# Performance work log

Measured on AMD Instinct MI355X. Metric: run time of the kernel, lower is better.

## Reference

```python
import jax, jax.numpy as jnp
import numpy as np

N = 768          # number of proposals (graph nodes)
C = 1024         # box_head feature dim (in_feats)
HC = 256         # RelPN hidden_c
K = 20           # topk edges per node
GH = 256         # gcn_hidden
H1 = 4           # gat1 heads
IMG_H, IMG_W = 800.0, 800.0
NEG_SLOPE = 0.2  # PyG GATConv leaky_relu slope


def setup_inputs() -> dict:
    key = jax.random.key(0)
    ks = jax.random.split(key, 24)
    s = 0.02
    feats = jax.random.normal(ks[0], (N, C), jnp.float32)
    # valid boxes inside an 800x800 image
    cx = jax.random.uniform(ks[1], (N,), minval=100.0, maxval=700.0)
    cy = jax.random.uniform(ks[2], (N,), minval=100.0, maxval=700.0)
    w = jax.random.uniform(ks[3], (N,), minval=10.0, maxval=200.0)
    h = jax.random.uniform(ks[4], (N,), minval=10.0, maxval=200.0)
    boxes = jnp.stack([cx - 0.5 * w, cy - 0.5 * h, cx + 0.5 * w, cy + 0.5 * h], axis=1)
    rn = lambda k, sh: jax.random.normal(k, sh, jnp.float32) * s
    return {
        'feats': feats, 'boxes': boxes,
        # RelationProposalNetwork: fc1(2C+4 -> HC), fc2(HC -> 1)
        'W1': rn(ks[5], (2 * C + 4, HC)), 'b1': jnp.zeros((HC,), jnp.float32),
        'W2': rn(ks[6], (HC, 1)), 'b2': jnp.zeros((1,), jnp.float32),
        # GATConv(C+4 -> GH, heads=4)
        'g1W': rn(ks[7], (C + 4, H1 * GH)), 'g1as': rn(ks[8], (H1, GH)),
        'g1ad': rn(ks[9], (H1, GH)), 'g1b': jnp.zeros((H1 * GH,), jnp.float32),
        # GATConv(GH*4 -> 2, heads=1)
        'g2W': rn(ks[10], (H1 * GH, 2)), 'g2as': rn(ks[11], (1, 2)),
        'g2ad': rn(ks[12], (1, 2)), 'g2b': jnp.zeros((2,), jnp.float32),
        'rW1': rn(ks[13], (H1 * GH + 4, GH // 2)), 'rb1': jnp.zeros((GH // 2,), jnp.float32),
        'rW2': rn(ks[14], (GH // 2, 4)), 'rb2': jnp.zeros((4,), jnp.float32),
    }


def _gat(xin, W, a_src, a_dst, bias, heads, feat, nbr):
    """PyG-style GATConv (eval mode, self-loops already in nbr). nbr: [N, K+1] src ids per dst."""
    n = xin.shape[0]
    xp = (xin @ W).reshape(n, heads, feat)              # [N,H,F]
    asrc = jnp.einsum('nhf,hf->nh', xp, a_src)          # [N,H]
    adst = jnp.einsum('nhf,hf->nh', xp, a_dst)          # [N,H]
    logits = jax.nn.leaky_relu(asrc[nbr] + adst[:, None, :], NEG_SLOPE)  # [N,K+1,H]
    alpha = jax.nn.softmax(logits, axis=1)              # softmax over incoming edges per dst
    out = jnp.einsum('nkh,nkhf->nhf', alpha, xp[nbr])   # gather + weighted aggregate
    return out.reshape(n, heads * feat) + bias


def reference(feats, boxes, W1, b1, W2, b2, g1W, g1as, g1ad, g1b,
              g2W, g2as, g2ad, g2b, rW1, rb1, rW2, rb2):
    n = feats.shape[0]
    scale = jnp.array([IMG_W, IMG_H, IMG_W, IMG_H], jnp.float32)
    geom = boxes / scale                                 # _box_geom: normalized coords
    x = jnp.concatenate([feats, geom], axis=1)           # [N, C+4]

    # --- RelationProposalNetwork: fc1(cat[f_i, f_j, |b_i - b_j|]) decomposed ---
    Wa, Wb, Wg = W1[:C], W1[C:2 * C], W1[2 * C:]
    fa = feats @ Wa                                      # i-part  [N,HC]
    fb = feats @ Wb                                      # j-part  [N,HC]
    gdiff = jnp.abs(boxes[:, None, :] - boxes[None, :, :])          # [N,N,4]
    h = jax.nn.relu(fa[:, None, :] + fb[None, :, :]
                    + jnp.einsum('ijd,dh->ijh', gdiff, Wg) + b1)    # [N,N,HC]
    rel = jnp.einsum('ijh,h->ij', h, W2[:, 0]) + b2[0]              # [N,N]

    # --- top-k edges per destination node (exclude self), plus self-loops ---
    rel_masked = jnp.where(jnp.eye(n, dtype=bool), -1e9, rel)
    _, nbr = jax.lax.top_k(rel_masked, K)                # [N,K] src j for each dst i
    nbr = jnp.concatenate([nbr, jnp.arange(n)[:, None]], axis=1)    # [N,K+1]

    # --- GAT propagation ---
    h1 = jax.nn.relu(_gat(x, g1W, g1as, g1ad, g1b, H1, GH, nbr))    # [N,1024]
    logits = _gat(h1, g2W, g2as, g2ad, g2b, 1, 2, nbr)              # [N,2]

    reg_in = jnp.concatenate([h1, geom], axis=1)
    delta = jax.nn.relu(reg_in @ rW1 + rb1) @ rW2 + rb2             # [N,4]
    px0, py0, px1, py1 = boxes[:, 0], boxes[:, 1], boxes[:, 2], boxes[:, 3]
    pw, ph = px1 - px0, py1 - py0
    pcx, pcy = px0 + 0.5 * pw, py0 + 0.5 * ph
    dx, dy, dw, dh = delta[:, 0], delta[:, 1], delta[:, 2], delta[:, 3]
    gcx, gcy = dx * pw + pcx, dy * ph + pcy
    gw, gh = jnp.exp(dw) * pw, jnp.exp(dh) * ph
    final_boxes = jnp.stack([gcx - 0.5 * gw, gcy - 0.5 * gh,
                             gcx + 0.5 * gw, gcy + 0.5 * gh], axis=1)
    return jnp.concatenate([logits, final_boxes], axis=1)  # [N,6]
```

## Files before the change

kernel.cpp:

```cpp
#include <hip/hip_runtime.h>
#include <math.h>

#define NN 768
#define KK_TOP 20
#define NBR_K 21

typedef __attribute__((ext_vector_type(8))) short bf16x8;
typedef __attribute__((ext_vector_type(4))) float f32x4;
typedef unsigned short ushort_t;
typedef unsigned int uint_t;

__device__ __forceinline__ ushort_t f2bf(float x) {
    union { float f; uint_t u; } c; c.f = x;
    uint_t r = (c.u + 0x7FFFu + ((c.u >> 16) & 1u)) >> 16;
    return (ushort_t)r;
}
__device__ __forceinline__ float bf2f(ushort_t u) {
    union { uint_t u; float f; } c; c.u = ((uint_t)u) << 16;
    return c.f;
}

struct Params {
    const float *feats, *boxes, *W1, *b1, *W2, *b2;
    const float *g1W, *g1as, *g1ad, *g1b, *g2W, *g2as, *g2ad, *g2b;
    const float *rW1, *rb1, *rW2, *rb2;
    float *out;
    float *fafb, *xp, *relm, *hid, *Arow, *Brow, *asrc, *adst, *xp2, *aux2;
    float4 *wgt4; float *w2p, *consts;
    float *va, *vb, *av;
    int *nbr;
    ushort_t *featsbf, *btAB, *btG, *btR, *h1bf;
};

__global__ __launch_bounds__(256) void k_prep(Params P)
{
    int b = blockIdx.x, t = threadIdx.x;
    if (b == 800) {
        const float* Wg = P.W1 + 2048 * 256;
        float q0 = Wg[t], q1 = Wg[256 + t], q2 = Wg[512 + t], q3 = Wg[768 + t];
        float w2 = P.W2[t];
        P.wgt4[t] = make_float4(q0, q1, q2, q3);
        P.w2p[t] = w2;
        __shared__ float red[256];
        float vals[5] = {q0 * w2, q1 * w2, q2 * w2, q3 * w2, P.b1[t] * w2};
        for (int d = 0; d < 5; d++) {
            red[t] = vals[d]; __syncthreads();
            for (int s = 128; s > 0; s >>= 1) {
                if (t < s) red[t] += red[t + s];
                __syncthreads();
            }
            if (t == 0) P.consts[d] = red[0];
            __syncthreads();
        }
        return;
    }
    if (b >= 1313) {
        int o = (b - 1313) * 4 + (t >> 6);
        int lane = t & 63;
        if (o >= 8224) return;
        int vec = o / 1028, k = o - vec * 1028;
        int h = vec & 3;
        const float4* aw = (const float4*)(((vec < 4) ? P.g1as : P.g1ad) + h * 256);
        const float4* gw = (const float4*)(P.g1W + (size_t)k * 1024 + h * 256);
        float4 a = aw[lane], g = gw[lane];
        float s = a.x * g.x + a.y * g.y + a.z * g.z + a.w * g.w;
#pragma unroll
        for (int off = 32; off > 0; off >>= 1) s += __shfl_xor(s, off);
        if (lane == 0) P.av[o] = s;
        return;
    }
    if (b >= 801) {
        int o = (b - 801) * 4 + (t >> 6);
        int lane = t & 63;
        const float4* row = (const float4*)(P.W1 + (size_t)o * 256);
        float4 w = ((const float4*)P.W2)[lane];
        float4 f = row[lane];
        float s = f.x * w.x + f.y * w.y + f.z * w.z + f.w * w.w;
#pragma unroll
        for (int off = 32; off > 0; off >>= 1) s += __shfl_xor(s, off);
        if (lane == 0) { if (o < 1024) P.va[o] = s; else P.vb[o - 1024] = s; }
        return;
    }
    if (b >= 416) {
        int gid = (b - 416) * 2048 + t * 8;
        float4 v0 = *(const float4*)(P.feats + gid);
        float4 v1 = *(const float4*)(P.feats + gid + 4);
        uint4 r;
        r.x = (uint_t)f2bf(v0.x) | ((uint_t)f2bf(v0.y) << 16);
        r.y = (uint_t)f2bf(v0.z) | ((uint_t)f2bf(v0.w) << 16);
        r.z = (uint_t)f2bf(v1.x) | ((uint_t)f2bf(v1.y) << 16);
        r.w = (uint_t)f2bf(v1.z) | ((uint_t)f2bf(v1.w) << 16);
        *(uint4*)(P.featsbf + gid) = r;
        return;
    }
    const float* in; ushort_t* out; int ldN, tk, tn;
    if (b < 64)       { in = P.W1;              out = P.btAB;              ldN = 256;  tn = b & 3;  tk = b >> 2; }
    else if (b < 128) { int i = b - 64;  in = P.W1 + 1024 * 256; out = P.btAB + 256 * 1024; ldN = 256;  tn = i & 3;  tk = i >> 2; }
    else if (b < 384) { int i = b - 128; in = P.g1W;             out = P.btG;               ldN = 1024; tn = i & 15; tk = i >> 4; }
    else              { int i = b - 384; in = P.rW1;             out = P.btR;               ldN = 128;  tn = i & 1;  tk = i >> 1; }

    __shared__ __align__(16) float tile[64][68];
    int k0 = tk * 64, n0 = tn * 64;
#pragma unroll
    for (int it = 0; it < 4; it++) {
        int r = (t >> 4) + it * 16;
        int c = (t & 15) * 4;
        *(float4*)&tile[r][c] = *(const float4*)(in + (size_t)(k0 + r) * ldN + n0 + c);
    }
    __syncthreads();
    int n = t >> 2;
    int kc = (t & 3) * 16;
    uint_t p[8];
#pragma unroll
    for (int h = 0; h < 8; h++) {
        ushort_t lo = f2bf(tile[kc + 2 * h][n]);
        ushort_t hi = f2bf(tile[kc + 2 * h + 1][n]);
        p[h] = (uint_t)lo | ((uint_t)hi << 16);
    }
    ushort_t* dst = out + (size_t)(n0 + n) * 1024 + k0 + kc;
    *(uint4*)dst = make_uint4(p[0], p[1], p[2], p[3]);
    *(uint4*)(dst + 8) = make_uint4(p[4], p[5], p[6], p[7]);
}

__device__ __forceinline__ void mfma_unit(
    int bx, int by, const ushort_t* __restrict__ A, const ushort_t* __restrict__ Bt,
    float* __restrict__ C, int ldc, int mode,
    const float* __restrict__ boxes, const float* __restrict__ Wgeo,
    const float* __restrict__ bias, int t, char* smem)
{
    ushort_t (*As)[72] = (ushort_t(*)[72])smem;
    ushort_t (*Bs)[72] = (ushort_t(*)[72])(smem + 64 * 72 * 2);
    int m0 = by * 64, n0 = bx * 64;
    int lane = t & 63, w = t >> 6;
    int quad = lane >> 4, ci = lane & 15;

    int r0 = t >> 3, q0 = t & 7;
    int r1 = (t + 256) >> 3, q1 = (t + 256) & 7;

    const ushort_t* Abase = A + (size_t)(m0 + r0) * 1024 + q0 * 8;
    const ushort_t* Abase1 = A + (size_t)(m0 + r1) * 1024 + q1 * 8;
    const ushort_t* Bbase = Bt + (size_t)(n0 + r0) * 1024 + q0 * 8;
    const ushort_t* Bbase1 = Bt + (size_t)(n0 + r1) * 1024 + q1 * 8;

    uint4 pa0 = *(const uint4*)(Abase);
    uint4 pa1 = *(const uint4*)(Abase1);
    uint4 pb0 = *(const uint4*)(Bbase);
    uint4 pb1 = *(const uint4*)(Bbase1);

    f32x4 acc[2][2];
    acc[0][0] = (f32x4){0.f, 0.f, 0.f, 0.f};
    acc[0][1] = (f32x4){0.f, 0.f, 0.f, 0.f};
    acc[1][0] = (f32x4){0.f, 0.f, 0.f, 0.f};
    acc[1][1] = (f32x4){0.f, 0.f, 0.f, 0.f};

    int arow = (w & 1) * 32 + ci;
    int brow = (w >> 1) * 32 + ci;

    for (int kt = 0; kt < 16; kt++) {
        *(uint4*)&As[r0][q0 * 8] = pa0;
        *(uint4*)&As[r1][q1 * 8] = pa1;
        *(uint4*)&Bs[r0][q0 * 8] = pb0;
        *(uint4*)&Bs[r1][q1 * 8] = pb1;
        __syncthreads();
        if (kt < 15) {
            int ko = (kt + 1) * 64;
            pa0 = *(const uint4*)(Abase + ko);
            pa1 = *(const uint4*)(Abase1 + ko);
            pb0 = *(const uint4*)(Bbase + ko);
            pb1 = *(const uint4*)(Bbase1 + ko);
        }
#pragma unroll
        for (int s = 0; s < 2; s++) {
            int kb = s * 32 + quad * 8;
            bf16x8 a0 = *(const bf16x8*)&As[arow][kb];
            bf16x8 a1 = *(const bf16x8*)&As[arow + 16][kb];
            bf16x8 b0 = *(const bf16x8*)&Bs[brow][kb];
            bf16x8 b1 = *(const bf16x8*)&Bs[brow + 16][kb];
            acc[0][0] = __builtin_amdgcn_mfma_f32_16x16x32_bf16(a0, b0, acc[0][0], 0, 0, 0);
            acc[0][1] = __builtin_amdgcn_mfma_f32_16x16x32_bf16(a0, b1, acc[0][1], 0, 0, 0);
            acc[1][0] = __builtin_amdgcn_mfma_f32_16x16x32_bf16(a1, b0, acc[1][0], 0, 0, 0);
            acc[1][1] = __builtin_amdgcn_mfma_f32_16x16x32_bf16(a1, b1, acc[1][1], 0, 0, 0);
        }
        __syncthreads();
    }

    const float inv800 = 1.0f / 800.0f;
#pragma unroll
    for (int ni = 0; ni < 2; ni++) {
        int col = n0 + (w >> 1) * 32 + ni * 16 + ci;
        float wg0 = 0.f, wg1 = 0.f, wg2 = 0.f, wg3 = 0.f, bv = 0.f;
        if (mode) {
            wg0 = Wgeo[col]; wg1 = Wgeo[ldc + col];
            wg2 = Wgeo[2 * ldc + col]; wg3 = Wgeo[3 * ldc + col];
            if (mode == 2) bv = bias[col];
        }
#pragma unroll
        for (int mi = 0; mi < 2; mi++) {
            int rbase = m0 + (w & 1) * 32 + mi * 16 + quad * 4;
#pragma unroll
            for (int reg = 0; reg < 4; reg++) {
                int row = rbase + reg;
                float v = acc[mi][ni][reg];
                if (mode) {
                    float4 bx4 = *(const float4*)(boxes + row * 4);
                    v += (bx4.x * wg0 + bx4.y * wg1 + bx4.z * wg2 + bx4.w * wg3) * inv800 + bv;
                    if (mode == 2) v = fmaxf(v, 0.f);
                }
                C[(size_t)row * ldc + col] = v;
            }
        }
    }
}

__global__ __launch_bounds__(256) void k_gemms(Params P)
{
    __shared__ __align__(16) char smem[18432];
    int u = blockIdx.x, t = threadIdx.x;
    if (u < 96) {
        mfma_unit(u & 7, u >> 3, P.featsbf, P.btAB, P.fafb, 512, 0,
                  nullptr, nullptr, nullptr, t, smem);
    } else if (u < 288) {
        int v = u - 96;
        mfma_unit(v & 15, v >> 4, P.featsbf, P.btG, P.xp, 1024, 1,
                  P.boxes, P.g1W + (size_t)1024 * 1024, nullptr, t, smem);
    } else if (u < 480) {
        int row = (u - 288) * 4 + (t >> 6);
        int lane = t & 63;
        const float4* fr = (const float4*)(P.feats + (size_t)row * 1024);
        const float4* va4 = (const float4*)P.va;
        const float4* vb4 = (const float4*)P.vb;
        float s1 = 0.f, s2 = 0.f;
#pragma unroll
        for (int it = 0; it < 4; it++) {
            int idx = it * 64 + lane;
            float4 f = fr[idx], a = va4[idx], b = vb4[idx];
            s1 += f.x * a.x + f.y * a.y + f.z * a.z + f.w * a.w;
            s2 += f.x * b.x + f.y * b.y + f.z * b.z + f.w * b.w;
        }
#pragma unroll
        for (int off = 32; off > 0; off >>= 1) {
            s1 += __shfl_xor(s1, off);
            s2 += __shfl_xor(s2, off);
        }
        if (lane == 0) { P.Arow[row] = s1; P.Brow[row] = s2; }
    } else {
        int pair = (u - 480) * 4 + (t >> 6);
        int lane = t & 63;
        int n = pair >> 2, h = pair & 3;
        const float4* fr = (const float4*)(P.feats + (size_t)n * 1024);
        const float* vs = P.av + h * 1028;
        const float* vd = P.av + (4 + h) * 1028;
        const float4* vs4 = (const float4*)vs;
        const float4* vd4 = (const float4*)vd;
        float s1 = 0.f, s2 = 0.f;
#pragma unroll
        for (int it = 0; it < 4; it++) {
            int idx = it * 64 + lane;
            float4 f = fr[idx], a = vs4[idx], b = vd4[idx];
            s1 += f.x * a.x + f.y * a.y + f.z * a.z + f.w * a.w;
            s2 += f.x * b.x + f.y * b.y + f.z * b.z + f.w * b.w;
        }
#pragma unroll
        for (int off = 32; off > 0; off >>= 1) {
            s1 += __shfl_xor(s1, off);
            s2 += __shfl_xor(s2, off);
        }
        if (lane == 0) {
            const float inv800 = 1.0f / 800.0f;
            float4 bx = *(const float4*)(P.boxes + n * 4);
            float g0 = bx.x * inv800, g1 = bx.y * inv800, g2 = bx.z * inv800, g3 = bx.w * inv800;
            s1 += g0 * vs[1024] + g1 * vs[1025] + g2 * vs[1026] + g3 * vs[1027];
            s2 += g0 * vd[1024] + g1 * vd[1025] + g2 * vd[1026] + g3 * vd[1027];
            P.asrc[n * 4 + h] = s1;
            P.adst[n * 4 + h] = s2;
        }
    }
}

#define REL_ACC(FA0, FA1, FB0, FB1, Q, W)                                           \
    {                                                                               \
        float v;                                                                    \
        v = FA0 + FB0;                                                              \
        v = fmaf(g00.x, Q.x, v); v = fmaf(g00.y, Q.y, v);                           \
        v = fmaf(g00.z, Q.z, v); v = fmaf(g00.w, Q.w, v);                           \
        acc00 = fmaf(fabsf(v), W, acc00);                                           \
        v = FA0 + FB1;                                                              \
        v = fmaf(g01.x, Q.x, v); v = fmaf(g01.y, Q.y, v);                           \
        v = fmaf(g01.z, Q.z, v); v = fmaf(g01.w, Q.w, v);                           \
        acc01 = fmaf(fabsf(v), W, acc01);                                           \
        v = FA1 + FB0;                                                              \
        v = fmaf(g10.x, Q.x, v); v = fmaf(g10.y, Q.y, v);                           \
        v = fmaf(g10.z, Q.z, v); v = fmaf(g10.w, Q.w, v);                           \
        acc10 = fmaf(fabsf(v), W, acc10);                                           \
        v = FA1 + FB1;                                                              \
        v = fmaf(g11.x, Q.x, v); v = fmaf(g11.y, Q.y, v);                           \
        v = fmaf(g11.z, Q.z, v); v = fmaf(g11.w, Q.w, v);                           \
        acc11 = fmaf(fabsf(v), W, acc11);                                           \
    }

__global__ __launch_bounds__(256) void k_rel(Params P)
{
    __shared__ __align__(16) float fas[32][68];
    __shared__ __align__(16) float fbs[32][68];
    int t = threadIdx.x;
    int u = blockIdx.x;
    int half = (u >= 576) ? 1 : 0;
    int ub = u - half * 576;
    int bx = ub % 24, by = ub / 24;
    int tx = t & 15, ty = t >> 4;
    int i0 = by * 32, j0 = bx * 32;
    int ia = i0 + ty, ib = i0 + ty + 16;
    int ja = j0 + tx, jb = j0 + tx + 16;

    float4 Bi0 = *(const float4*)(P.boxes + ia * 4);
    float4 Bi1 = *(const float4*)(P.boxes + ib * 4);
    float4 Bj0 = *(const float4*)(P.boxes + ja * 4);
    float4 Bj1 = *(const float4*)(P.boxes + jb * 4);
    float4 g00 = make_float4(fabsf(Bi0.x - Bj0.x), fabsf(Bi0.y - Bj0.y), fabsf(Bi0.z - Bj0.z), fabsf(Bi0.w - Bj0.w));
    float4 g01 = make_float4(fabsf(Bi0.x - Bj1.x), fabsf(Bi0.y - Bj1.y), fabsf(Bi0.z - Bj1.z), fabsf(Bi0.w - Bj1.w));
    float4 g10 = make_float4(fabsf(Bi1.x - Bj0.x), fabsf(Bi1.y - Bj0.y), fabsf(Bi1.z - Bj0.z), fabsf(Bi1.w - Bj0.w));
    float4 g11 = make_float4(fabsf(Bi1.x - Bj1.x), fabsf(Bi1.y - Bj1.y), fabsf(Bi1.z - Bj1.z), fabsf(Bi1.w - Bj1.w));

    float acc00 = 0.f, acc01 = 0.f, acc10 = 0.f, acc11 = 0.f;

    for (int pp = 0; pp < 2; pp++) {
        int p = half * 2 + pp;
        for (int e = t; e < 512; e += 256) {
            int r = e >> 4, cq = e & 15;
            float4 bb = *(const float4*)(P.b1 + p * 64 + cq * 4);
            float4 fv = *(const float4*)(P.fafb + (size_t)(i0 + r) * 512 + p * 64 + cq * 4);
            float4 gv = *(const float4*)(P.fafb + (size_t)(j0 + r) * 512 + 256 + p * 64 + cq * 4);
            *(float4*)&fas[r][cq * 4] = make_float4(fv.x + bb.x, fv.y + bb.y, fv.z + bb.z, fv.w + bb.w);
            *(float4*)&fbs[r][cq * 4] = gv;
        }
        __syncthreads();
        const float4* wg = P.wgt4 + p * 64;
        const float* w2 = P.w2p + p * 64;
#pragma unroll 8
        for (int hc = 0; hc < 16; hc++) {
            int h4 = hc * 4;
            float4 fa0 = *(const float4*)&fas[ty][h4];
            float4 fa1 = *(const float4*)&fas[ty + 16][h4];
            float4 fb0 = *(const float4*)&fbs[tx][h4];
            float4 fb1 = *(const float4*)&fbs[tx + 16][h4];
            float4 w2v = *(const float4*)(w2 + h4);
            float4 q0 = wg[h4], q1 = wg[h4 + 1], q2 = wg[h4 + 2], q3 = wg[h4 + 3];
            REL_ACC(fa0.x, fa1.x, fb0.x, fb1.x, q0, w2v.x);
            REL_ACC(fa0.y, fa1.y, fb0.y, fb1.y, q1, w2v.y);
            REL_ACC(fa0.z, fa1.z, fb0.z, fb1.z, q2, w2v.z);
            REL_ACC(fa0.w, fa1.w, fb0.w, fb1.w, q3, w2v.w);
        }
        __syncthreads();
    }

    float* relh = P.relm + (size_t)half * NN * NN;
    if (half == 0) {
        float c0 = P.consts[0], c1 = P.consts[1], c2 = P.consts[2], c3 = P.consts[3], c4 = P.consts[4];
        float b2v = P.b2[0];
        float Ai0 = P.Arow[ia], Ai1 = P.Arow[ib];
        float Bja = P.Brow[ja], Bjb = P.Brow[jb];
        float lin, r00, r01, r10, r11;
        lin = Ai0 + Bja + g00.x * c0 + g00.y * c1 + g00.z * c2 + g00.w * c3 + c4;
        r00 = 0.5f * (lin + acc00) + b2v;
        lin = Ai0 + Bjb + g01.x * c0 + g01.y * c1 + g01.z * c2 + g01.w * c3 + c4;
        r01 = 0.5f * (lin + acc01) + b2v;
        lin = Ai1 + Bja + g10.x * c0 + g10.y * c1 + g10.z * c2 + g10.w * c3 + c4;
        r10 = 0.5f * (lin + acc10) + b2v;
        lin = Ai1 + Bjb + g11.x * c0 + g11.y * c1 + g11.z * c2 + g11.w * c3 + c4;
        r11 = 0.5f * (lin + acc11) + b2v;
        relh[(size_t)ia * NN + ja] = (ia == ja) ? -1e9f : r00;
        relh[(size_t)ia * NN + jb] = (ia == jb) ? -1e9f : r01;
        relh[(size_t)ib * NN + ja] = (ib == ja) ? -1e9f : r10;
        relh[(size_t)ib * NN + jb] = (ib == jb) ? -1e9f : r11;
    } else {
        relh[(size_t)ia * NN + ja] = (ia == ja) ? 0.f : 0.5f * acc00;
        relh[(size_t)ia * NN + jb] = (ia == jb) ? 0.f : 0.5f * acc01;
        relh[(size_t)ib * NN + ja] = (ib == ja) ? 0.f : 0.5f * acc10;
        relh[(size_t)ib * NN + jb] = (ib == jb) ? 0.f : 0.5f * acc11;
    }
}

__global__ __launch_bounds__(256) void k_topkgat1(Params P)
{
    int n = blockIdx.x, t = threadIdx.x;
    __shared__ int nb[NBR_K];
    __shared__ float alpha[NBR_K][4];

    if (t < 64) {
        int lane = t;
        const float* rp0 = P.relm + (size_t)n * NN;
        const float* rp1 = P.relm + (size_t)NN * NN + (size_t)n * NN;
        float v[12];
#pragma unroll
        for (int q = 0; q < 12; q++) v[q] = rp0[q * 64 + lane] + rp1[q * 64 + lane];
        for (int kk = 0; kk < KK_TOP; kk++) {
            float best = v[0]; int bq = 0;
#pragma unroll
            for (int q = 1; q < 12; q++) {
                if (v[q] > best) { best = v[q]; bq = q; }
            }
            int bidx = bq * 64 + lane;
#pragma unroll
            for (int off = 32; off > 0; off >>= 1) {
                float ov = __shfl_xor(best, off);
                int oi = __shfl_xor(bidx, off);
                if (ov > best || (ov == best && oi < bidx)) { best = ov; bidx = oi; }
            }
            if (lane == 0) { nb[kk] = bidx; P.nbr[n * NBR_K + kk] = bidx; }
            int bl = bidx & 63, bq2 = bidx >> 6;
            if (lane == bl) {
#pragma unroll
                for (int q = 0; q < 12; q++)
                    if (q == bq2) v[q] = -INFINITY;
            }
        }
        if (lane == 0) { nb[KK_TOP] = n; P.nbr[n * NBR_K + KK_TOP] = n; }
    }
    __syncthreads();

    if (t < NBR_K * 4) {
        int k = t % NBR_K, h = t / NBR_K;
        float e = P.asrc[nb[k] * 4 + h] + P.adst[n * 4 + h];
        e = (e > 0.f) ? e : 0.2f * e;
        alpha[k][h] = e;
    }
    __syncthreads();
    if (t < 4) {
        float m = -INFINITY;
        for (int k = 0; k < NBR_K; k++) m = fmaxf(m, alpha[k][t]);
        float s = 0.f;
        for (int k = 0; k < NBR_K; k++) { float ex = expf(alpha[k][t] - m); alpha[k][t] = ex; s += ex; }
        float inv = 1.f / s;
        for (int k = 0; k < NBR_K; k++) alpha[k][t] *= inv;
    }
    __syncthreads();

    int h = t >> 6;
    float ax = 0.f, ay = 0.f, az = 0.f, aw = 0.f;
#pragma unroll 7
    for (int k = 0; k < NBR_K; k++) {
        float a = alpha[k][h];
        float4 xv = ((const float4*)(P.xp + (size_t)nb[k] * 1024))[t];
        ax = fmaf(a, xv.x, ax); ay = fmaf(a, xv.y, ay);
        az = fmaf(a, xv.z, az); aw = fmaf(a, xv.w, aw);
    }
    float4 gb = ((const float4*)P.g1b)[t];
    uint2 pk;
    pk.x = (uint_t)f2bf(fmaxf(ax + gb.x, 0.f)) | ((uint_t)f2bf(fmaxf(ay + gb.y, 0.f)) << 16);
    pk.y = (uint_t)f2bf(fmaxf(az + gb.z, 0.f)) | ((uint_t)f2bf(fmaxf(aw + gb.w, 0.f)) << 16);
    *(uint2*)(P.h1bf + (size_t)n * 1024 + t * 4) = pk;
}

__global__ __launch_bounds__(256) void k_p6(Params P)
{
    __shared__ __align__(16) char smem[18432];
    int u = blockIdx.x, t = threadIdx.x;
    if (u < 192) {
        int wid = u * 4 + (t >> 6);
        int lane = t & 63;
        float s0 = 0.f, s1 = 0.f;
#pragma unroll
        for (int it = 0; it < 4; it++) {
            int k = it * 256 + lane * 4;
            uint2 pk = *(const uint2*)(P.h1bf + (size_t)wid * 1024 + k);
            float v0 = bf2f((ushort_t)(pk.x & 0xFFFF));
            float v1 = bf2f((ushort_t)(pk.x >> 16));
            float v2 = bf2f((ushort_t)(pk.y & 0xFFFF));
            float v3 = bf2f((ushort_t)(pk.y >> 16));
            float4 w0 = *(const float4*)(P.g2W + k * 2);
            float4 w1 = *(const float4*)(P.g2W + k * 2 + 4);
            s0 += v0 * w0.x + v1 * w0.z + v2 * w1.x + v3 * w1.z;
            s1 += v0 * w0.y + v1 * w0.w + v2 * w1.y + v3 * w1.w;
        }
#pragma unroll
        for (int off = 32; off > 0; off >>= 1) { s0 += __shfl_down(s0, off); s1 += __shfl_down(s1, off); }
        if (lane == 0) {
            P.xp2[wid * 2 + 0] = s0; P.xp2[wid * 2 + 1] = s1;
            P.aux2[wid * 2 + 0] = s0 * P.g2as[0] + s1 * P.g2as[1];
            P.aux2[wid * 2 + 1] = s0 * P.g2ad[0] + s1 * P.g2ad[1];
        }
    } else {
        int v = u - 192;
        mfma_unit(v & 1, v >> 1, P.h1bf, P.btR, P.hid, 128, 2,
                  P.boxes, P.rW1 + (size_t)1024 * 128, P.rb1, t, smem);
    }
}

__global__ __launch_bounds__(256) void k_p7(Params P)
{
    __shared__ __align__(16) float rw2s[512];
    int u = blockIdx.x, t = threadIdx.x;
    if (u < 192) {
        int n = u * 4 + (t >> 6);
        int lane = t & 63;
        float adstv = P.aux2[n * 2 + 1];
        float e = -INFINITY, x0 = 0.f, x1 = 0.f;
        if (lane < NBR_K) {
            int nbk = P.nbr[n * NBR_K + lane];
            float vv = P.aux2[nbk * 2 + 0] + adstv;
            e = (vv > 0.f) ? vv : 0.2f * vv;
            x0 = P.xp2[nbk * 2 + 0];
            x1 = P.xp2[nbk * 2 + 1];
        }
        float m = e;
#pragma unroll
        for (int off = 32; off > 0; off >>= 1) m = fmaxf(m, __shfl_xor(m, off));
        float ex = (lane < NBR_K) ? expf(e - m) : 0.f;
        float ssum = ex, o0 = ex * x0, o1 = ex * x1;
#pragma unroll
        for (int off = 32; off > 0; off >>= 1) {
            ssum += __shfl_xor(ssum, off);
            o0 += __shfl_xor(o0, off);
            o1 += __shfl_xor(o1, off);
        }
        if (lane == 0) {
            float inv = 1.f / ssum;
            P.out[n * 6 + 0] = o0 * inv + P.g2b[0];
            P.out[n * 6 + 1] = o1 * inv + P.g2b[1];
        }
        return;
    }
    *(float2*)&rw2s[t * 2] = *(const float2*)(P.rW2 + t * 2);
    __syncthreads();
    int n = (u - 192) * 256 + t;
    const float4* hrow = (const float4*)(P.hid + (size_t)n * 128);
    float d0 = 0.f, d1 = 0.f, d2 = 0.f, d3 = 0.f;
#pragma unroll 8
    for (int k4 = 0; k4 < 32; k4++) {
        float4 h = hrow[k4];
        const float* wv = &rw2s[k4 * 16];
        d0 = fmaf(h.x, wv[0], d0);  d1 = fmaf(h.x, wv[1], d1);
        d2 = fmaf(h.x, wv[2], d2);  d3 = fmaf(h.x, wv[3], d3);
        d0 = fmaf(h.y, wv[4], d0);  d1 = fmaf(h.y, wv[5], d1);
        d2 = fmaf(h.y, wv[6], d2);  d3 = fmaf(h.y, wv[7], d3);
        d0 = fmaf(h.z, wv[8], d0);  d1 = fmaf(h.z, wv[9], d1);
        d2 = fmaf(h.z, wv[10], d2); d3 = fmaf(h.z, wv[11], d3);
        d0 = fmaf(h.w, wv[12], d0); d1 = fmaf(h.w, wv[13], d1);
        d2 = fmaf(h.w, wv[14], d2); d3 = fmaf(h.w, wv[15], d3);
    }
    d0 += P.rb2[0]; d1 += P.rb2[1]; d2 += P.rb2[2]; d3 += P.rb2[3];
    float4 bx = *(const float4*)(P.boxes + n * 4);
    float pw = bx.z - bx.x, ph = bx.w - bx.y;
    float pcx = bx.x + 0.5f * pw, pcy = bx.y + 0.5f * ph;
    float gcx = d0 * pw + pcx, gcy = d1 * ph + pcy;
    float gw = expf(d2) * pw, gh = expf(d3) * ph;
    P.out[n * 6 + 2] = gcx - 0.5f * gw;
    P.out[n * 6 + 3] = gcy - 0.5f * gh;
    P.out[n * 6 + 4] = gcx + 0.5f * gw;
    P.out[n * 6 + 5] = gcy + 0.5f * gh;
}

extern "C" void kernel_launch(void* const* d_in, const int* in_sizes, int n_in,
                              void* d_out, int out_size, void* d_ws, size_t ws_size,
                              hipStream_t stream)
{
    Params P;
    P.feats = (const float*)d_in[0];
    P.boxes = (const float*)d_in[1];
    P.W1    = (const float*)d_in[2];
    P.b1    = (const float*)d_in[3];
    P.W2    = (const float*)d_in[4];
    P.b2    = (const float*)d_in[5];
    P.g1W   = (const float*)d_in[6];
    P.g1as  = (const float*)d_in[7];
    P.g1ad  = (const float*)d_in[8];
    P.g1b   = (const float*)d_in[9];
    P.g2W   = (const float*)d_in[10];
    P.g2as  = (const float*)d_in[11];
    P.g2ad  = (const float*)d_in[12];
    P.g2b   = (const float*)d_in[13];
    P.rW1   = (const float*)d_in[14];
    P.rb1   = (const float*)d_in[15];
    P.rW2   = (const float*)d_in[16];
    P.rb2   = (const float*)d_in[17];
    P.out   = (float*)d_out;

    float* ws = (float*)d_ws;
    P.fafb  = ws;
    P.xp    = P.fafb + 393216;
    P.relm  = P.xp + 786432;
    P.hid   = P.relm + 2 * 589824;
    P.Arow  = P.hid + 98304;
    P.Brow  = P.Arow + 768;
    P.asrc  = P.Brow + 768;
    P.adst  = P.asrc + 3072;
    P.xp2   = P.adst + 3072;
    P.aux2  = P.xp2 + 1536;
    P.wgt4  = (float4*)(P.aux2 + 1536);
    P.w2p   = (float*)(P.wgt4 + 256);
    P.consts= P.w2p + 256;
    P.va    = P.consts + 8;
    P.vb    = P.va + 1024;
    P.av    = P.vb + 1024;
    P.nbr   = (int*)(P.av + 8224);
    P.featsbf = (ushort_t*)(P.nbr + 16128);
    P.btAB    = P.featsbf + 786432;
    P.btG     = P.btAB + 524288;
    P.btR     = P.btG + 1048576;
    P.h1bf    = P.btR + 131072;

    k_prep    <<<dim3(3369), dim3(256), 0, stream>>>(P);
    k_gemms   <<<dim3(1248), dim3(256), 0, stream>>>(P);
    k_rel     <<<dim3(1152), dim3(256), 0, stream>>>(P);
    k_topkgat1<<<dim3(768),  dim3(256), 0, stream>>>(P);
    k_p6      <<<dim3(216),  dim3(256), 0, stream>>>(P);
    k_p7      <<<dim3(195),  dim3(256), 0, stream>>>(P);
}
```

Before: 176.8 us.

## Split relation kernel into four hidden-chunk partials and fuse GAT2 projection into topk-GAT1

The relation-score kernel now splits the hidden dimension four ways instead of two, launching twice as many blocks that each handle one 64-wide chunk and write a separate partial matrix. The top-k kernel sums all four partials. The GAT2 input projection (h1·g2W and the attention dot products) moves into the topk/GAT1 kernel, reusing the fp32 h1 values already in registers, so k_p6 only runs the regressor MFMA blocks. This raises parallelism and removes one reread of h1. In exchange it adds workspace, extra partial-matrix traffic and extra top-k loads.

```diff
diff --git a/kernel.cpp b/kernel.cpp
--- a/kernel.cpp
+++ b/kernel.cpp
@@ -304,8 +304,8 @@
     __shared__ __align__(16) float fbs[32][68];
     int t = threadIdx.x;
     int u = blockIdx.x;
-    int half = (u >= 576) ? 1 : 0;
-    int ub = u - half * 576;
+    int quarter = u / 576;
+    int ub = u - quarter * 576;
     int bx = ub % 24, by = ub / 24;
     int tx = t & 15, ty = t >> 4;
     int i0 = by * 32, j0 = bx * 32;
@@ -323,38 +323,35 @@
 
     float acc00 = 0.f, acc01 = 0.f, acc10 = 0.f, acc11 = 0.f;
 
-    for (int pp = 0; pp < 2; pp++) {
-        int p = half * 2 + pp;
-        for (int e = t; e < 512; e += 256) {
-            int r = e >> 4, cq = e & 15;
-            float4 bb = *(const float4*)(P.b1 + p * 64 + cq * 4);
-            float4 fv = *(const float4*)(P.fafb + (size_t)(i0 + r) * 512 + p * 64 + cq * 4);
-            float4 gv = *(const float4*)(P.fafb + (size_t)(j0 + r) * 512 + 256 + p * 64 + cq * 4);
-            *(float4*)&fas[r][cq * 4] = make_float4(fv.x + bb.x, fv.y + bb.y, fv.z + bb.z, fv.w + bb.w);
-            *(float4*)&fbs[r][cq * 4] = gv;
-        }
-        __syncthreads();
-        const float4* wg = P.wgt4 + p * 64;
-        const float* w2 = P.w2p + p * 64;
+    int p = quarter;
+    for (int e = t; e < 512; e += 256) {
+        int r = e >> 4, cq = e & 15;
+        float4 bb = *(const float4*)(P.b1 + p * 64 + cq * 4);
+        float4 fv = *(const float4*)(P.fafb + (size_t)(i0 + r) * 512 + p * 64 + cq * 4);
+        float4 gv = *(const float4*)(P.fafb + (size_t)(j0 + r) * 512 + 256 + p * 64 + cq * 4);
+        *(float4*)&fas[r][cq * 4] = make_float4(fv.x + bb.x, fv.y + bb.y, fv.z + bb.z, fv.w + bb.w);
+        *(float4*)&fbs[r][cq * 4] = gv;
+    }
+    __syncthreads();
+    const float4* wg = P.wgt4 + p * 64;
+    const float* w2 = P.w2p + p * 64;
 #pragma unroll 8
-        for (int hc = 0; hc < 16; hc++) {
-            int h4 = hc * 4;
-            float4 fa0 = *(const float4*)&fas[ty][h4];
-            float4 fa1 = *(const float4*)&fas[ty + 16][h4];
-            float4 fb0 = *(const float4*)&fbs[tx][h4];
-            float4 fb1 = *(const float4*)&fbs[tx + 16][h4];
-            float4 w2v = *(const float4*)(w2 + h4);
-            float4 q0 = wg[h4], q1 = wg[h4 + 1], q2 = wg[h4 + 2], q3 = wg[h4 + 3];
-            REL_ACC(fa0.x, fa1.x, fb0.x, fb1.x, q0, w2v.x);
-            REL_ACC(fa0.y, fa1.y, fb0.y, fb1.y, q1, w2v.y);
-            REL_ACC(fa0.z, fa1.z, fb0.z, fb1.z, q2, w2v.z);
-            REL_ACC(fa0.w, fa1.w, fb0.w, fb1.w, q3, w2v.w);
-        }
-        __syncthreads();
-    }
-
-    float* relh = P.relm + (size_t)half * NN * NN;
-    if (half == 0) {
+    for (int hc = 0; hc < 16; hc++) {
+        int h4 = hc * 4;
+        float4 fa0 = *(const float4*)&fas[ty][h4];
+        float4 fa1 = *(const float4*)&fas[ty + 16][h4];
+        float4 fb0 = *(const float4*)&fbs[tx][h4];
+        float4 fb1 = *(const float4*)&fbs[tx + 16][h4];
+        float4 w2v = *(const float4*)(w2 + h4);
+        float4 q0 = wg[h4], q1 = wg[h4 + 1], q2 = wg[h4 + 2], q3 = wg[h4 + 3];
+        REL_ACC(fa0.x, fa1.x, fb0.x, fb1.x, q0, w2v.x);
+        REL_ACC(fa0.y, fa1.y, fb0.y, fb1.y, q1, w2v.y);
+        REL_ACC(fa0.z, fa1.z, fb0.z, fb1.z, q2, w2v.z);
+        REL_ACC(fa0.w, fa1.w, fb0.w, fb1.w, q3, w2v.w);
+    }
+
+    float* relh = P.relm + (size_t)quarter * NN * NN;
+    if (quarter == 0) {
         float c0 = P.consts[0], c1 = P.consts[1], c2 = P.consts[2], c3 = P.consts[3], c4 = P.consts[4];
         float b2v = P.b2[0];
         float Ai0 = P.Arow[ia], Ai1 = P.Arow[ib];
@@ -385,14 +382,18 @@
     int n = blockIdx.x, t = threadIdx.x;
     __shared__ int nb[NBR_K];
     __shared__ float alpha[NBR_K][4];
+    __shared__ float red2[8];
 
     if (t < 64) {
         int lane = t;
         const float* rp0 = P.relm + (size_t)n * NN;
-        const float* rp1 = P.relm + (size_t)NN * NN + (size_t)n * NN;
+        const float* rp1 = rp0 + (size_t)NN * NN;
+        const float* rp2 = rp1 + (size_t)NN * NN;
+        const float* rp3 = rp2 + (size_t)NN * NN;
         float v[12];
 #pragma unroll
-        for (int q = 0; q < 12; q++) v[q] = rp0[q * 64 + lane] + rp1[q * 64 + lane];
+        for (int q = 0; q < 12; q++)
+            v[q] = (rp0[q * 64 + lane] + rp1[q * 64 + lane]) + (rp2[q * 64 + lane] + rp3[q * 64 + lane]);
         for (int kk = 0; kk < KK_TOP; kk++) {
             float best = v[0]; int bq = 0;
 #pragma unroll
@@ -445,45 +446,39 @@
         az = fmaf(a, xv.z, az); aw = fmaf(a, xv.w, aw);
     }
     float4 gb = ((const float4*)P.g1b)[t];
+    float hv0 = fmaxf(ax + gb.x, 0.f), hv1 = fmaxf(ay + gb.y, 0.f);
+    float hv2 = fmaxf(az + gb.z, 0.f), hv3 = fmaxf(aw + gb.w, 0.f);
     uint2 pk;
-    pk.x = (uint_t)f2bf(fmaxf(ax + gb.x, 0.f)) | ((uint_t)f2bf(fmaxf(ay + gb.y, 0.f)) << 16);
-    pk.y = (uint_t)f2bf(fmaxf(az + gb.z, 0.f)) | ((uint_t)f2bf(fmaxf(aw + gb.w, 0.f)) << 16);
+    pk.x = (uint_t)f2bf(hv0) | ((uint_t)f2bf(hv1) << 16);
+    pk.y = (uint_t)f2bf(hv2) | ((uint_t)f2bf(hv3) << 16);
     *(uint2*)(P.h1bf + (size_t)n * 1024 + t * 4) = pk;
+
+    float4 w0 = *(const float4*)(P.g2W + t * 8);
+    float4 w1 = *(const float4*)(P.g2W + t * 8 + 4);
+    float s0 = hv0 * w0.x + hv1 * w0.z + hv2 * w1.x + hv3 * w1.z;
+    float s1 = hv0 * w0.y + hv1 * w0.w + hv2 * w1.y + hv3 * w1.w;
+#pragma unroll
+    for (int off = 32; off > 0; off >>= 1) {
+        s0 += __shfl_xor(s0, off);
+        s1 += __shfl_xor(s1, off);
+    }
+    if ((t & 63) == 0) { red2[(t >> 6) * 2] = s0; red2[(t >> 6) * 2 + 1] = s1; }
+    __syncthreads();
+    if (t == 0) {
+        float S0 = red2[0] + red2[2] + red2[4] + red2[6];
+        float S1 = red2[1] + red2[3] + red2[5] + red2[7];
+        P.xp2[n * 2 + 0] = S0; P.xp2[n * 2 + 1] = S1;
+        P.aux2[n * 2 + 0] = S0 * P.g2as[0] + S1 * P.g2as[1];
+        P.aux2[n * 2 + 1] = S0 * P.g2ad[0] + S1 * P.g2ad[1];
+    }
 }
 
 __global__ __launch_bounds__(256) void k_p6(Params P)
 {
     __shared__ __align__(16) char smem[18432];
-    int u = blockIdx.x, t = threadIdx.x;
-    if (u < 192) {
-        int wid = u * 4 + (t >> 6);
-        int lane = t & 63;
-        float s0 = 0.f, s1 = 0.f;
-#pragma unroll
-        for (int it = 0; it < 4; it++) {
-            int k = it * 256 + lane * 4;
-            uint2 pk = *(const uint2*)(P.h1bf + (size_t)wid * 1024 + k);
-            float v0 = bf2f((ushort_t)(pk.x & 0xFFFF));
-            float v1 = bf2f((ushort_t)(pk.x >> 16));
-            float v2 = bf2f((ushort_t)(pk.y & 0xFFFF));
-            float v3 = bf2f((ushort_t)(pk.y >> 16));
-            float4 w0 = *(const float4*)(P.g2W + k * 2);
-            float4 w1 = *(const float4*)(P.g2W + k * 2 + 4);
-            s0 += v0 * w0.x + v1 * w0.z + v2 * w1.x + v3 * w1.z;
-            s1 += v0 * w0.y + v1 * w0.w + v2 * w1.y + v3 * w1.w;
-        }
-#pragma unroll
-        for (int off = 32; off > 0; off >>= 1) { s0 += __shfl_down(s0, off); s1 += __shfl_down(s1, off); }
-        if (lane == 0) {
-            P.xp2[wid * 2 + 0] = s0; P.xp2[wid * 2 + 1] = s1;
-            P.aux2[wid * 2 + 0] = s0 * P.g2as[0] + s1 * P.g2as[1];
-            P.aux2[wid * 2 + 1] = s0 * P.g2ad[0] + s1 * P.g2ad[1];
-        }
-    } else {
-        int v = u - 192;
-        mfma_unit(v & 1, v >> 1, P.h1bf, P.btR, P.hid, 128, 2,
-                  P.boxes, P.rW1 + (size_t)1024 * 128, P.rb1, t, smem);
-    }
+    int v = blockIdx.x, t = threadIdx.x;
+    mfma_unit(v & 1, v >> 1, P.h1bf, P.btR, P.hid, 128, 2,
+              P.boxes, P.rW1 + (size_t)1024 * 128, P.rb1, t, smem);
 }
 
 __global__ __launch_bounds__(256) void k_p7(Params P)
@@ -579,7 +574,7 @@
     P.fafb  = ws;
     P.xp    = P.fafb + 393216;
     P.relm  = P.xp + 786432;
-    P.hid   = P.relm + 2 * 589824;
+    P.hid   = P.relm + 4 * 589824;
     P.Arow  = P.hid + 98304;
     P.Brow  = P.Arow + 768;
     P.asrc  = P.Brow + 768;
@@ -601,8 +596,8 @@
 
     k_prep    <<<dim3(3369), dim3(256), 0, stream>>>(P);
     k_gemms   <<<dim3(1248), dim3(256), 0, stream>>>(P);
-    k_rel     <<<dim3(1152), dim3(256), 0, stream>>>(P);
+    k_rel     <<<dim3(2304), dim3(256), 0, stream>>>(P);
     k_topkgat1<<<dim3(768),  dim3(256), 0, stream>>>(P);
-    k_p6      <<<dim3(216),  dim3(256), 0, stream>>>(P);
+    k_p6      <<<dim3(24),   dim3(256), 0, stream>>>(P);
     k_p7      <<<dim3(195),  dim3(256), 0, stream>>>(P);
 }
```

Result: slower. 182.8 us (+3.4%).
